# Kernel tuning notes

Measured on AMD Instinct MI355X. Metric: run time of the kernel, lower is better.

## Reference

```python
import math
import jax, jax.numpy as jnp
import numpy as np

B, N, D = 16, 2048, 64

def setup_inputs() -> dict:
    key = jax.random.key(0)
    kq, kk, kv, kl = jax.random.split(key, 4)
    q = jax.random.normal(kq, (B, N, D), dtype=jnp.float32)
    k = jax.random.normal(kk, (B, N, D), dtype=jnp.float32)
    v = jax.random.normal(kv, (B, N, D), dtype=jnp.float32)
    valid = jax.random.randint(kl, (B, N), 0, 2048, dtype=jnp.int64 if jax.config.jax_enable_x64 else jnp.int32)
    return {"q": q, "k": k, "v": v, "valid": valid}

def reference(q, k, v, valid):
    # scores[b,i,j] = <q[b,i], k[b,j]> / sqrt(d)
    d = k.shape[-1]
    scores = jnp.einsum('bid,bjd->bij', q, k) / jnp.sqrt(jnp.asarray(d, q.dtype))
    # mask[b,i,j] = (j+1) > valid[b,i]; masked positions replaced by 1e-6
    # (faithful to torch.masked_fill(scores, mask, 1e-06) -- NOT -inf)
    key_pos = jnp.arange(1, scores.shape[-1] + 1)  # [N]
    mask = key_pos[None, None, :] > valid[:, :, None]  # [B,N,N]
    mask_scores = jnp.where(mask, jnp.asarray(1e-06, scores.dtype), scores)
    weights = jax.nn.softmax(mask_scores, axis=-1)
    # dropout p=0.0 -> identity
    return jnp.einsum('bij,bjd->bid', weights, v)
```

## Files before the change

### kernel.cpp

```cpp
#include <hip/hip_runtime.h>
#include <hip/hip_bf16.h>
#include <stdint.h>

#define BB 16
#define NN 2048
#define DD 64
#define BM 128
#define BN 64
#define KSTR 72
#define PSTR 72

typedef __attribute__((ext_vector_type(8))) short short8;
typedef __attribute__((ext_vector_type(4))) float f32x4;
typedef __attribute__((ext_vector_type(2))) unsigned int uint32x2_t;
typedef __attribute__((ext_vector_type(4))) unsigned int uint32x4_t;

__device__ __forceinline__ unsigned short f2bf(float f) {
  union { float f; uint32_t u; } c; c.f = f;
  uint32_t u = c.u + 0x7fffu + ((c.u >> 16) & 1u);
  return (unsigned short)(u >> 16);
}
__device__ __forceinline__ uint32_t pkrn(float a, float b) {
  union { __hip_bfloat162 h; uint32_t u; } c;
  c.h = __float22bfloat162_rn(make_float2(a, b));
  return c.u;
}

#define QSCALE 0.18033688f
#define CMW 1.0000010f

__global__ __launch_bounds__(256) void prep_kernel(const float* __restrict__ v,
                                                   const int* __restrict__ valid,
                                                   unsigned short* __restrict__ vt,
                                                   int* __restrict__ perm,
                                                   int* __restrict__ sval,
                                                   float* __restrict__ tsum,
                                                   int* __restrict__ cnt) {
  __shared__ float t[64][65];
  __shared__ int hist[2048];
  __shared__ int part[256];
  int id = blockIdx.x, tid = threadIdx.x;
  if (id < 512) {
    int b = id >> 5;
    int k0 = (id & 31) * 64;
    const float4* src = (const float4*)(v + ((size_t)b * NN + k0) * DD);
#pragma unroll
    for (int i = 0; i < 4; i++) {
      int f4 = tid + i * 256;
      int row = f4 >> 4, c4 = f4 & 15;
      float4 f = src[f4];
      t[row][c4*4+0] = f.x; t[row][c4*4+1] = f.y; t[row][c4*4+2] = f.z; t[row][c4*4+3] = f.w;
    }
    __syncthreads();
    int d = tid >> 2, kg = tid & 3;
    unsigned short* dst = vt + ((size_t)b * DD + d) * NN + k0 + kg * 16;
#pragma unroll
    for (int u = 0; u < 4; u++) {
      ushort4 o;
      o.x = f2bf(t[kg*16+u*4+0][d]);
      o.y = f2bf(t[kg*16+u*4+1][d]);
      o.z = f2bf(t[kg*16+u*4+2][d]);
      o.w = f2bf(t[kg*16+u*4+3][d]);
      ((ushort4*)dst)[u] = o;
    }
    if (tid < 64) {
      float s0 = 0.0f, s1 = 0.0f, s2 = 0.0f, s3 = 0.0f;
#pragma unroll 4
      for (int kk = 0; kk < 64; kk += 4) {
        s0 += t[kk+0][tid]; s1 += t[kk+1][tid];
        s2 += t[kk+2][tid]; s3 += t[kk+3][tid];
      }
      tsum[((size_t)b * 32 + (k0 >> 6)) * 64 + tid] = (s0 + s1) + (s2 + s3);
    }
  } else {
    int b = id - 512;
    if (tid < 16) cnt[(b << 4) | tid] = 0;
    for (int i = tid; i < 2048; i += 256) hist[i] = 0;
    __syncthreads();
    for (int i = tid; i < NN; i += 256) atomicAdd(&hist[valid[b * NN + i]], 1);
    __syncthreads();
    int base = tid * 8, loc[8], s = 0;
#pragma unroll
    for (int j = 0; j < 8; j++) { loc[j] = s; s += hist[base + j]; }
    int lane6 = tid & 63, wv = tid >> 6;
    int val = s;
#pragma unroll
    for (int off = 1; off < 64; off <<= 1) {
      int n = __shfl_up(val, off);
      if (lane6 >= off) val += n;
    }
    if (lane6 == 63) part[wv] = val;
    __syncthreads();
    int add = 0;
    for (int i = 0; i < wv; i++) add += part[i];
    int excl = (val - s) + add;
    __syncthreads();
#pragma unroll
    for (int j = 0; j < 8; j++) hist[base + j] = excl + loc[j];
    __syncthreads();
    for (int i = tid; i < NN; i += 256) {
      int vv = valid[b * NN + i];
      int pos = atomicAdd(&hist[vv], 1);
      perm[b * NN + pos] = i;
      sval[b * NN + pos] = vv;
    }
  }
}

template <int NS>
__global__ __launch_bounds__(512, 4) void attn_kernel(
    const float* __restrict__ q, const float* __restrict__ k,
    const unsigned short* __restrict__ vtbf, const int* __restrict__ perm,
    const int* __restrict__ sval, const float* __restrict__ tsum,
    float* __restrict__ out, unsigned short* __restrict__ po,
    float* __restrict__ pz, int* __restrict__ cnt)
{
  constexpr int NT = 32 / NS;

  __shared__ __align__(16) unsigned short Klds[BN * KSTR];
  __shared__ __align__(16) unsigned short Vlds[DD * KSTR];
  __shared__ __align__(16) unsigned short Plds[8 * 16 * PSTR];
  __shared__ int vld[BM];
  __shared__ int pidx[BM];
  __shared__ int lastFlag;

  int id = blockIdx.x;
  int b = (id & 7) + 8 * ((id >> 3) & 1);
  int rest = id >> 4;
  int sp = rest % NS;
  int u = 15 - rest / NS;
  int i0 = u * BM;

  int tid = threadIdx.x;
  int w = tid >> 6, lane = tid & 63;
  int m = lane & 15, quad = lane >> 4;
  int h = w >> 2, wq = w & 3;
  int row = h * 64 + wq * 16 + m;

  if (tid < BM) {
    vld[tid]  = sval[b * NN + i0 + tid];
    pidx[tid] = perm[b * NN + i0 + tid];
  }
  int Th = (sval[b * NN + i0 + h * 64 + 63] + 63) >> 6;
  int T1 = (sval[b * NN + i0 + 127] + 63) >> 6;
  int nh     = (Th - sp + NS - 1) / NS;
  int nstage = (T1 - sp + NS - 1) / NS;

  __syncthreads();

  f32x4 o[4] = {{0,0,0,0},{0,0,0,0},{0,0,0,0},{0,0,0,0}};
  float z = 0.0f;

  if (nstage > 0) {
    int vq = vld[row];
    int qrow = pidx[row];

    short8 qf[2];
    {
      const float* qp = q + ((size_t)b * NN + qrow) * DD;
#pragma unroll
      for (int s = 0; s < 2; s++) {
        float4 f0 = *(const float4*)(qp + s * 32 + quad * 8);
        float4 f1 = *(const float4*)(qp + s * 32 + quad * 8 + 4);
        union { short8 v; uint32_t x[4]; } tmp;
        tmp.x[0] = pkrn(f0.x * QSCALE, f0.y * QSCALE);
        tmp.x[1] = pkrn(f0.z * QSCALE, f0.w * QSCALE);
        tmp.x[2] = pkrn(f1.x * QSCALE, f1.y * QSCALE);
        tmp.x[3] = pkrn(f1.z * QSCALE, f1.w * QSCALE);
        qf[s] = tmp.v;
      }
    }

    unsigned short* pbase = Plds + w * 16 * PSTR;
    int srow = tid >> 3, scol = (tid & 7) * 8;
    const float* gk = k + ((size_t)(b * NN + sp * BN + srow)) * DD + scol;
    const unsigned short* gv = vtbf + ((size_t)b * DD + srow) * NN + sp * BN + scol;

    float4 ka0 = *(const float4*)gk, ka1 = *(const float4*)(gk + 4);
    uint4 va = *(const uint4*)gv;

    for (int it = 0; it < nstage; ++it) {
      int j0 = (sp + NS * it) * BN;
      __syncthreads();
      *(uint4*)&Klds[srow * KSTR + scol] =
          make_uint4(pkrn(ka0.x, ka0.y), pkrn(ka0.z, ka0.w),
                     pkrn(ka1.x, ka1.y), pkrn(ka1.z, ka1.w));
      *(uint4*)&Vlds[srow * KSTR + scol] = va;
      if (it + 1 < nstage) {
        gk += (size_t)NS * BN * DD; gv += NS * BN;
        ka0 = *(const float4*)gk; ka1 = *(const float4*)(gk + 4);
        va = *(const uint4*)gv;
      }
      __syncthreads();

      if (it < nh) {
        f32x4 s[4] = {{0,0,0,0},{0,0,0,0},{0,0,0,0},{0,0,0,0}};
#pragma unroll
        for (int c = 0; c < 4; c++) {
#pragma unroll
          for (int ss = 0; ss < 2; ss++) {
            short8 kf = *(const short8*)&Klds[(c * 16 + m) * KSTR + ss * 32 + quad * 8];
            s[c] = __builtin_amdgcn_mfma_f32_16x16x32_bf16(kf, qf[ss], s[c], 0, 0, 0);
          }
        }

#pragma unroll
        for (int c = 0; c < 4; c++) {
          float e[4];
#pragma unroll
          for (int rr = 0; rr < 4; rr++) {
            int j = j0 + c * 16 + quad * 4 + rr;
            float ex = __builtin_amdgcn_exp2f(s[c][rr]);
            e[rr] = (j < vq) ? ex : CMW;
          }
          z += (e[0] + e[1]) + (e[2] + e[3]);
          *(uint2*)&pbase[m * PSTR + c * 16 + quad * 4] =
              make_uint2(pkrn(e[0], e[1]), pkrn(e[2], e[3]));
        }

        __builtin_amdgcn_s_waitcnt(0xc07f);

#pragma unroll
        for (int ss = 0; ss < 2; ss++) {
          short8 pf = *(const short8*)&pbase[m * PSTR + ss * 32 + quad * 8];
#pragma unroll
          for (int t = 0; t < 4; t++) {
            short8 vf = *(const short8*)&Vlds[(t * 16 + m) * KSTR + ss * 32 + quad * 8];
            o[t] = __builtin_amdgcn_mfma_f32_16x16x32_bf16(vf, pf, o[t], 0, 0, 0);
          }
        }
      }
    }
  }

  z += __shfl_xor(z, 16);
  z += __shfl_xor(z, 32);
  z += CMW * (float)((NT - nh) * 64);

  {
    const float* tb = tsum + (size_t)b * 32 * 64;
    for (int i = nh; i < NT; ++i) {
      const float* tr = tb + (sp + NS * i) * 64;
#pragma unroll
      for (int t = 0; t < 4; t++) {
        float4 a = *(const float4*)&tr[t * 16 + quad * 4];
        o[t][0] += CMW * a.x;
        o[t][1] += CMW * a.y;
        o[t][2] += CMW * a.z;
        o[t][3] += CMW * a.w;
      }
    }
  }

  if (NS > 1) {
    int rrow = i0 + row;
    unsigned short* op = po + ((size_t)((sp * BB + b) * NN) + rrow) * DD;
#pragma unroll
    for (int t = 0; t < 4; t++) {
      uint32x2_t wv2 = {pkrn(o[t][0], o[t][1]), pkrn(o[t][2], o[t][3])};
      asm volatile("global_store_dwordx2 %0, %1, off sc0 sc1"
                   :: "v"(op + t * 16 + quad * 4), "v"(wv2) : "memory");
    }
    if (quad == 0) {
      float* pzp = pz + (size_t)(sp * BB + b) * NN + rrow;
      asm volatile("global_store_dword %0, %1, off sc0 sc1"
                   :: "v"(pzp), "v"(z) : "memory");
    }
    asm volatile("s_waitcnt vmcnt(0)" ::: "memory");
    __syncthreads();
    if (tid == 0) {
      int old = atomicAdd(&cnt[(b << 4) | u], 1);
      lastFlag = (old == NS - 1);
    }
    __syncthreads();
    if (lastFlag) {
      for (int item = tid; item < BM * 8; item += 512) {
        int r = item >> 3, g = item & 7;
        int rrow2 = i0 + r;
        float acc[8] = {0,0,0,0,0,0,0,0};
        float zs = 0.0f;
        if constexpr (NS == 4) {
          const unsigned short* p0 = po + ((size_t)((0 * BB + b) * NN) + rrow2) * DD + g * 8;
          const unsigned short* p1 = po + ((size_t)((1 * BB + b) * NN) + rrow2) * DD + g * 8;
          const unsigned short* p2 = po + ((size_t)((2 * BB + b) * NN) + rrow2) * DD + g * 8;
          const unsigned short* p3 = po + ((size_t)((3 * BB + b) * NN) + rrow2) * DD + g * 8;
          const float* q0 = pz + (size_t)(0 * BB + b) * NN + rrow2;
          const float* q1 = pz + (size_t)(1 * BB + b) * NN + rrow2;
          const float* q2 = pz + (size_t)(2 * BB + b) * NN + rrow2;
          const float* q3 = pz + (size_t)(3 * BB + b) * NN + rrow2;
          uint32x4_t a0, a1, a2, a3; float z0, z1, z2, z3;
          asm volatile(
            "global_load_dwordx4 %0, %8, off sc0 sc1\n\t"
            "global_load_dwordx4 %1, %9, off sc0 sc1\n\t"
            "global_load_dwordx4 %2, %10, off sc0 sc1\n\t"
            "global_load_dwordx4 %3, %11, off sc0 sc1\n\t"
            "global_load_dword %4, %12, off sc0 sc1\n\t"
            "global_load_dword %5, %13, off sc0 sc1\n\t"
            "global_load_dword %6, %14, off sc0 sc1\n\t"
            "global_load_dword %7, %15, off sc0 sc1\n\t"
            "s_waitcnt vmcnt(0)"
            : "=&v"(a0), "=&v"(a1), "=&v"(a2), "=&v"(a3),
              "=&v"(z0), "=&v"(z1), "=&v"(z2), "=&v"(z3)
            : "v"(p0), "v"(p1), "v"(p2), "v"(p3),
              "v"(q0), "v"(q1), "v"(q2), "v"(q3)
            : "memory");
          zs = ((z0 + z1) + (z2 + z3));
          uint32_t aw[4][4] = {{a0.x, a0.y, a0.z, a0.w}, {a1.x, a1.y, a1.z, a1.w},
                               {a2.x, a2.y, a2.z, a2.w}, {a3.x, a3.y, a3.z, a3.w}};
#pragma unroll
          for (int s2 = 0; s2 < 4; s2++)
#pragma unroll
            for (int i = 0; i < 4; i++) {
              acc[2*i]   += __uint_as_float(aw[s2][i] << 16);
              acc[2*i+1] += __uint_as_float(aw[s2][i] & 0xffff0000u);
            }
        } else {
          for (int s2 = 0; s2 < NS; s2++) {
            const unsigned short* pp = po + ((size_t)((s2 * BB + b) * NN) + rrow2) * DD + g * 8;
            uint32x4_t a; float zv;
            asm volatile("global_load_dwordx4 %0, %2, off sc0 sc1\n\t"
                         "global_load_dword %1, %3, off sc0 sc1\n\t"
                         "s_waitcnt vmcnt(0)"
                         : "=&v"(a), "=&v"(zv)
                         : "v"(pp), "v"(pz + (size_t)(s2 * BB + b) * NN + rrow2)
                         : "memory");
            zs += zv;
            uint32_t aw[4] = {a.x, a.y, a.z, a.w};
#pragma unroll
            for (int i = 0; i < 4; i++) {
              acc[2*i]   += __uint_as_float(aw[i] << 16);
              acc[2*i+1] += __uint_as_float(aw[i] & 0xffff0000u);
            }
          }
        }
        float inv = 1.0f / zs;
        float* opf = out + ((size_t)b * NN + pidx[r]) * DD + g * 8;
        *(float4*)&opf[0] = make_float4(acc[0]*inv, acc[1]*inv, acc[2]*inv, acc[3]*inv);
        *(float4*)&opf[4] = make_float4(acc[4]*inv, acc[5]*inv, acc[6]*inv, acc[7]*inv);
      }
    }
  } else {
    float inv = 1.0f / z;
    int qrow = pidx[row];
    float* op2 = out + ((size_t)b * NN + qrow) * DD;
#pragma unroll
    for (int t = 0; t < 4; t++)
      *(float4*)&op2[t * 16 + quad * 4] =
          make_float4(o[t][0]*inv, o[t][1]*inv, o[t][2]*inv, o[t][3]*inv);
  }
}

extern "C" void kernel_launch(void* const* d_in, const int* in_sizes, int n_in,
                              void* d_out, int out_size, void* d_ws, size_t ws_size,
                              hipStream_t stream) {
  const float* q = (const float*)d_in[0];
  const float* k = (const float*)d_in[1];
  const float* v = (const float*)d_in[2];
  const int* valid = (const int*)d_in[3];
  float* out = (float*)d_out;

  unsigned short* vtbf = (unsigned short*)d_ws;
  int*   perm = (int*)(vtbf + (size_t)BB * NN * DD);
  int*   sv   = perm + (size_t)BB * NN;
  float* tsum = (float*)(sv + (size_t)BB * NN);
  int*   cnt  = (int*)(tsum + (size_t)BB * 32 * DD);
  float* pz   = (float*)(cnt + 256);
  unsigned short* po = (unsigned short*)(pz + (size_t)4 * BB * NN);

  size_t need4 = ((char*)(po + (size_t)4 * BB * NN * DD)) - (char*)d_ws;

  hipLaunchKernelGGL(prep_kernel, dim3(528), dim3(256), 0, stream,
                     v, valid, vtbf, perm, sv, tsum, cnt);
  if (ws_size >= need4) {
    hipLaunchKernelGGL((attn_kernel<4>), dim3(16 * 16 * 4), dim3(512), 0, stream,
                       q, k, vtbf, perm, sv, tsum, out, po, pz, cnt);
  } else {
    hipLaunchKernelGGL((attn_kernel<1>), dim3(16 * 16), dim3(512), 0, stream,
                       q, k, vtbf, perm, sv, tsum, out, po, pz, cnt);
  }
}
```

Before: 109.8 us.

## Double-buffer K/V tiles, halve key splits, and merge partials in registers

```diff
diff --git a/kernel.cpp b/kernel.cpp
--- a/kernel.cpp
+++ b/kernel.cpp
@@ -13,7 +13,6 @@
 typedef __attribute__((ext_vector_type(8))) short short8;
 typedef __attribute__((ext_vector_type(4))) float f32x4;
 typedef __attribute__((ext_vector_type(2))) unsigned int uint32x2_t;
-typedef __attribute__((ext_vector_type(4))) unsigned int uint32x4_t;
 
 __device__ __forceinline__ unsigned short f2bf(float f) {
   union { float f; uint32_t u; } c; c.f = f;
@@ -40,9 +39,10 @@
   __shared__ int hist[2048];
   __shared__ int part[256];
   int id = blockIdx.x, tid = threadIdx.x;
-  if (id < 512) {
-    int b = id >> 5;
-    int k0 = (id & 31) * 64;
+  if (id >= 16) {
+    int bid = id - 16;
+    int b = bid >> 5;
+    int k0 = (bid & 31) * 64;
     const float4* src = (const float4*)(v + ((size_t)b * NN + k0) * DD);
 #pragma unroll
     for (int i = 0; i < 4; i++) {
@@ -73,7 +73,7 @@
       tsum[((size_t)b * 32 + (k0 >> 6)) * 64 + tid] = (s0 + s1) + (s2 + s3);
     }
   } else {
-    int b = id - 512;
+    int b = id;
     if (tid < 16) cnt[(b << 4) | tid] = 0;
     for (int i = tid; i < 2048; i += 256) hist[i] = 0;
     __syncthreads();
@@ -117,8 +117,8 @@
 {
   constexpr int NT = 32 / NS;
 
-  __shared__ __align__(16) unsigned short Klds[BN * KSTR];
-  __shared__ __align__(16) unsigned short Vlds[DD * KSTR];
+  __shared__ __align__(16) unsigned short Klds[2][BN * KSTR];
+  __shared__ __align__(16) unsigned short Vlds[2][DD * KSTR];
   __shared__ __align__(16) unsigned short Plds[8 * 16 * PSTR];
   __shared__ int vld[BM];
   __shared__ int pidx[BM];
@@ -179,27 +179,40 @@
     float4 ka0 = *(const float4*)gk, ka1 = *(const float4*)(gk + 4);
     uint4 va = *(const uint4*)gv;
 
+    *(uint4*)&Klds[0][srow * KSTR + scol] =
+        make_uint4(pkrn(ka0.x, ka0.y), pkrn(ka0.z, ka0.w),
+                   pkrn(ka1.x, ka1.y), pkrn(ka1.z, ka1.w));
+    *(uint4*)&Vlds[0][srow * KSTR + scol] = va;
+    if (nstage > 1) {
+      gk += (size_t)NS * BN * DD; gv += NS * BN;
+      ka0 = *(const float4*)gk; ka1 = *(const float4*)(gk + 4);
+      va = *(const uint4*)gv;
+    }
+    __syncthreads();
+
     for (int it = 0; it < nstage; ++it) {
-      int j0 = (sp + NS * it) * BN;
-      __syncthreads();
-      *(uint4*)&Klds[srow * KSTR + scol] =
-          make_uint4(pkrn(ka0.x, ka0.y), pkrn(ka0.z, ka0.w),
-                     pkrn(ka1.x, ka1.y), pkrn(ka1.z, ka1.w));
-      *(uint4*)&Vlds[srow * KSTR + scol] = va;
+      int cur = it & 1;
       if (it + 1 < nstage) {
-        gk += (size_t)NS * BN * DD; gv += NS * BN;
-        ka0 = *(const float4*)gk; ka1 = *(const float4*)(gk + 4);
-        va = *(const uint4*)gv;
-      }
-      __syncthreads();
+        int nxt = cur ^ 1;
+        *(uint4*)&Klds[nxt][srow * KSTR + scol] =
+            make_uint4(pkrn(ka0.x, ka0.y), pkrn(ka0.z, ka0.w),
+                       pkrn(ka1.x, ka1.y), pkrn(ka1.z, ka1.w));
+        *(uint4*)&Vlds[nxt][srow * KSTR + scol] = va;
+        if (it + 2 < nstage) {
+          gk += (size_t)NS * BN * DD; gv += NS * BN;
+          ka0 = *(const float4*)gk; ka1 = *(const float4*)(gk + 4);
+          va = *(const uint4*)gv;
+        }
+      }
 
       if (it < nh) {
+        int j0 = (sp + NS * it) * BN;
         f32x4 s[4] = {{0,0,0,0},{0,0,0,0},{0,0,0,0},{0,0,0,0}};
 #pragma unroll
         for (int c = 0; c < 4; c++) {
 #pragma unroll
           for (int ss = 0; ss < 2; ss++) {
-            short8 kf = *(const short8*)&Klds[(c * 16 + m) * KSTR + ss * 32 + quad * 8];
+            short8 kf = *(const short8*)&Klds[cur][(c * 16 + m) * KSTR + ss * 32 + quad * 8];
             s[c] = __builtin_amdgcn_mfma_f32_16x16x32_bf16(kf, qf[ss], s[c], 0, 0, 0);
           }
         }
@@ -225,11 +238,12 @@
           short8 pf = *(const short8*)&pbase[m * PSTR + ss * 32 + quad * 8];
 #pragma unroll
           for (int t = 0; t < 4; t++) {
-            short8 vf = *(const short8*)&Vlds[(t * 16 + m) * KSTR + ss * 32 + quad * 8];
+            short8 vf = *(const short8*)&Vlds[cur][(t * 16 + m) * KSTR + ss * 32 + quad * 8];
             o[t] = __builtin_amdgcn_mfma_f32_16x16x32_bf16(vf, pf, o[t], 0, 0, 0);
           }
         }
       }
+      __syncthreads();
     }
   }
 
@@ -254,12 +268,12 @@
 
   if (NS > 1) {
     int rrow = i0 + row;
-    unsigned short* op = po + ((size_t)((sp * BB + b) * NN) + rrow) * DD;
+    unsigned short* op = po + ((size_t)((sp * BB + b) * NN) + rrow) * DD + quad * 4;
 #pragma unroll
     for (int t = 0; t < 4; t++) {
       uint32x2_t wv2 = {pkrn(o[t][0], o[t][1]), pkrn(o[t][2], o[t][3])};
       asm volatile("global_store_dwordx2 %0, %1, off sc0 sc1"
-                   :: "v"(op + t * 16 + quad * 4), "v"(wv2) : "memory");
+                   :: "v"(op + t * 16), "v"(wv2) : "memory");
     }
     if (quad == 0) {
       float* pzp = pz + (size_t)(sp * BB + b) * NN + rrow;
@@ -274,70 +288,39 @@
     }
     __syncthreads();
     if (lastFlag) {
-      for (int item = tid; item < BM * 8; item += 512) {
-        int r = item >> 3, g = item & 7;
-        int rrow2 = i0 + r;
-        float acc[8] = {0,0,0,0,0,0,0,0};
-        float zs = 0.0f;
-        if constexpr (NS == 4) {
-          const unsigned short* p0 = po + ((size_t)((0 * BB + b) * NN) + rrow2) * DD + g * 8;
-          const unsigned short* p1 = po + ((size_t)((1 * BB + b) * NN) + rrow2) * DD + g * 8;
-          const unsigned short* p2 = po + ((size_t)((2 * BB + b) * NN) + rrow2) * DD + g * 8;
-          const unsigned short* p3 = po + ((size_t)((3 * BB + b) * NN) + rrow2) * DD + g * 8;
-          const float* q0 = pz + (size_t)(0 * BB + b) * NN + rrow2;
-          const float* q1 = pz + (size_t)(1 * BB + b) * NN + rrow2;
-          const float* q2 = pz + (size_t)(2 * BB + b) * NN + rrow2;
-          const float* q3 = pz + (size_t)(3 * BB + b) * NN + rrow2;
-          uint32x4_t a0, a1, a2, a3; float z0, z1, z2, z3;
-          asm volatile(
-            "global_load_dwordx4 %0, %8, off sc0 sc1\n\t"
-            "global_load_dwordx4 %1, %9, off sc0 sc1\n\t"
-            "global_load_dwordx4 %2, %10, off sc0 sc1\n\t"
-            "global_load_dwordx4 %3, %11, off sc0 sc1\n\t"
-            "global_load_dword %4, %12, off sc0 sc1\n\t"
-            "global_load_dword %5, %13, off sc0 sc1\n\t"
-            "global_load_dword %6, %14, off sc0 sc1\n\t"
-            "global_load_dword %7, %15, off sc0 sc1\n\t"
-            "s_waitcnt vmcnt(0)"
-            : "=&v"(a0), "=&v"(a1), "=&v"(a2), "=&v"(a3),
-              "=&v"(z0), "=&v"(z1), "=&v"(z2), "=&v"(z3)
-            : "v"(p0), "v"(p1), "v"(p2), "v"(p3),
-              "v"(q0), "v"(q1), "v"(q2), "v"(q3)
-            : "memory");
-          zs = ((z0 + z1) + (z2 + z3));
-          uint32_t aw[4][4] = {{a0.x, a0.y, a0.z, a0.w}, {a1.x, a1.y, a1.z, a1.w},
-                               {a2.x, a2.y, a2.z, a2.w}, {a3.x, a3.y, a3.z, a3.w}};
-#pragma unroll
-          for (int s2 = 0; s2 < 4; s2++)
-#pragma unroll
-            for (int i = 0; i < 4; i++) {
-              acc[2*i]   += __uint_as_float(aw[s2][i] << 16);
-              acc[2*i+1] += __uint_as_float(aw[s2][i] & 0xffff0000u);
-            }
-        } else {
-          for (int s2 = 0; s2 < NS; s2++) {
-            const unsigned short* pp = po + ((size_t)((s2 * BB + b) * NN) + rrow2) * DD + g * 8;
-            uint32x4_t a; float zv;
-            asm volatile("global_load_dwordx4 %0, %2, off sc0 sc1\n\t"
-                         "global_load_dword %1, %3, off sc0 sc1\n\t"
-                         "s_waitcnt vmcnt(0)"
-                         : "=&v"(a), "=&v"(zv)
-                         : "v"(pp), "v"(pz + (size_t)(s2 * BB + b) * NN + rrow2)
-                         : "memory");
-            zs += zv;
-            uint32_t aw[4] = {a.x, a.y, a.z, a.w};
-#pragma unroll
-            for (int i = 0; i < 4; i++) {
-              acc[2*i]   += __uint_as_float(aw[i] << 16);
-              acc[2*i+1] += __uint_as_float(aw[i] & 0xffff0000u);
-            }
-          }
-        }
-        float inv = 1.0f / zs;
-        float* opf = out + ((size_t)b * NN + pidx[r]) * DD + g * 8;
-        *(float4*)&opf[0] = make_float4(acc[0]*inv, acc[1]*inv, acc[2]*inv, acc[3]*inv);
-        *(float4*)&opf[4] = make_float4(acc[4]*inv, acc[5]*inv, acc[6]*inv, acc[7]*inv);
-      }
+      float zs = z;
+#pragma unroll
+      for (int s2 = 0; s2 < NS; s2++) {
+        if (s2 == sp) continue;
+        const unsigned short* pp = po + ((size_t)((s2 * BB + b) * NN) + rrow) * DD + quad * 4;
+        const float* pzp2 = pz + (size_t)(s2 * BB + b) * NN + rrow;
+        uint32x2_t a0, a1, a2, a3; float zv;
+        asm volatile(
+          "global_load_dwordx2 %0, %5, off sc0 sc1\n\t"
+          "global_load_dwordx2 %1, %6, off sc0 sc1\n\t"
+          "global_load_dwordx2 %2, %7, off sc0 sc1\n\t"
+          "global_load_dwordx2 %3, %8, off sc0 sc1\n\t"
+          "global_load_dword %4, %9, off sc0 sc1\n\t"
+          "s_waitcnt vmcnt(0)"
+          : "=&v"(a0), "=&v"(a1), "=&v"(a2), "=&v"(a3), "=&v"(zv)
+          : "v"(pp), "v"(pp + 16), "v"(pp + 32), "v"(pp + 48), "v"(pzp2)
+          : "memory");
+        zs += zv;
+        uint32_t aw[4][2] = {{a0.x,a0.y},{a1.x,a1.y},{a2.x,a2.y},{a3.x,a3.y}};
+#pragma unroll
+        for (int t = 0; t < 4; t++) {
+          o[t][0] += __uint_as_float(aw[t][0] << 16);
+          o[t][1] += __uint_as_float(aw[t][0] & 0xffff0000u);
+          o[t][2] += __uint_as_float(aw[t][1] << 16);
+          o[t][3] += __uint_as_float(aw[t][1] & 0xffff0000u);
+        }
+      }
+      float inv = 1.0f / zs;
+      float* op2 = out + ((size_t)b * NN + pidx[row]) * DD + quad * 4;
+#pragma unroll
+      for (int t = 0; t < 4; t++)
+        *(float4*)&op2[t * 16] =
+            make_float4(o[t][0]*inv, o[t][1]*inv, o[t][2]*inv, o[t][3]*inv);
     }
   } else {
     float inv = 1.0f / z;
@@ -365,14 +348,14 @@
   float* tsum = (float*)(sv + (size_t)BB * NN);
   int*   cnt  = (int*)(tsum + (size_t)BB * 32 * DD);
   float* pz   = (float*)(cnt + 256);
-  unsigned short* po = (unsigned short*)(pz + (size_t)4 * BB * NN);
-
-  size_t need4 = ((char*)(po + (size_t)4 * BB * NN * DD)) - (char*)d_ws;
+  unsigned short* po = (unsigned short*)(pz + (size_t)2 * BB * NN);
+
+  size_t need2 = ((char*)(po + (size_t)2 * BB * NN * DD)) - (char*)d_ws;
 
   hipLaunchKernelGGL(prep_kernel, dim3(528), dim3(256), 0, stream,
                      v, valid, vtbf, perm, sv, tsum, cnt);
-  if (ws_size >= need4) {
-    hipLaunchKernelGGL((attn_kernel<4>), dim3(16 * 16 * 4), dim3(512), 0, stream,
+  if (ws_size >= need2) {
+    hipLaunchKernelGGL((attn_kernel<2>), dim3(16 * 16 * 2), dim3(512), 0, stream,
                        q, k, vtbf, perm, sv, tsum, out, po, pz, cnt);
   } else {
     hipLaunchKernelGGL((attn_kernel<1>), dim3(16 * 16), dim3(512), 0, stream,
```

New measurement: 109.4 us. No clear change (-0.4%).
